# Performance work log

Measured on AMD Instinct MI355X. Metric: run time of the kernel, lower is better.

The kernel has to match this reference:

```python
import jax, jax.numpy as jnp
import numpy as np

H = 0.01      # RK4 step size (parameter.h)
LAM = 1.0     # stage-cost gate penalty
R_COST = 0.1  # scalar control cost R
WMIN, WMAX = -0.01, 0.01  # disturbance range
B, N_STATES, T_STEPS = 8192, 2, 2048

# substituted plant dynamics (parameter.x1_dot / parameter.x2_dot)
def _x1_dot(x1, x2, u):
    return -2.0 * x1 + x2 + u

def _x2_dot(x1, x2, u):
    return x1 - 2.0 * x2 + u

def _rk4_step(x, u):
    # Faithful to RungeKutta.f: k2 == k3 (both evaluated at x2 + h/2)
    x1, x2 = x[0], x[1]
    k1 = jnp.stack([_x1_dot(x1, x2, u), _x2_dot(x1, x2, u)])
    k2 = jnp.stack([_x1_dot(x1, x2 + H / 2, u), _x2_dot(x1, x2 + H / 2, u)])
    k4 = jnp.stack([_x1_dot(x1, x2 + H, u), _x2_dot(x1, x2 + H, u)])
    return x + H * (k1 + 4.0 * k2 + k4) / 6.0  # (k1+2k2+2k3+k4)/6 with k3=k2


def setup_inputs() -> dict:
    key = jax.random.key(0)
    kw, kK, kL, kM, kMo = jax.random.split(key, 5)
    w = jax.random.uniform(kw, (B, N_STATES, T_STEPS), dtype=jnp.float32,
                           minval=WMIN, maxval=WMAX)
    K = 0.1 * jax.random.normal(kK, (1, N_STATES), dtype=jnp.float32)
    L = 0.05 * jax.random.normal(kL, (2 * N_STATES, 2 * N_STATES), dtype=jnp.float32)
    M = 0.05 * jax.random.normal(kM, (1, 2 * N_STATES), dtype=jnp.float32)
    Mo = 0.05 * jax.random.normal(kMo, (1, 1), dtype=jnp.float32)
    return {"w": w, "K": K, "L": L, "M": M, "Mo": Mo}


def reference(w, K, L, M, Mo):
    # w: (B, N, T) disturbances; returns per-sample trajectory cost J, shape (B,)
    Bsz, N, T = w.shape
    dt = w.dtype
    Q = jnp.eye(N, dtype=dt)
    Qf = 10.0 * jnp.eye(N, dtype=dt)
    x0 = jnp.zeros((N,), dtype=dt).at[0].set(1.0)  # xf = 0
    steps = jnp.arange(T)

    def traj_cost(w_b):  # w_b: (N, T)
        def step(carry, inp):
            x, x_hat = carry          # each (N,)
            w_t, i = inp
            z = jnp.concatenate([x, x_hat])            # phi input (2N,)
            phi = z @ L @ z + M[0] @ z + Mo[0, 0]
            delta = jnp.where(i == 0, jnp.asarray(1.0, dt), jax.nn.sigmoid(phi))
            x_hat_n = jnp.where(i == 0, x_hat, delta * x + (1.0 - delta) * x_hat)
            u = K[0] @ x_hat_n                         # control from gated estimate
            x_next = _rk4_step(x, u) + w_t
            u_s = K[0] @ x                             # J uses K @ x[:,i]
            sc = x @ Q @ x + R_COST * u_s * u_s + LAM * delta
            return (x_next, x_hat_n), sc

        (x_T, _), scs = jax.lax.scan(step, (x0, x0), (w_b.T, steps))
        return jnp.sum(scs[: T - 1]) + x_T @ Qf @ x_T

    return jax.vmap(traj_cost)(w)
```

## Files before the change

kernel.cpp:

```cpp
#include <hip/hip_runtime.h>


#define T_STEPS 2048
#define BATCH   8192

__global__ __launch_bounds__(64, 1) void cstr_kernel(
    const float* __restrict__ w,
    const float* __restrict__ K,
    const float* __restrict__ L,
    const float* __restrict__ M,
    const float* __restrict__ Mo,
    float* __restrict__ out)
{
    const int s = blockIdx.x * 64 + (int)threadIdx.x;

    constexpr float Hs = 0.01f;
    constexpr float Ad = 1.0f - 2.0f * Hs;
    constexpr float Rc = 0.1f;
    constexpr float SC = -1.44269504088896340736f;

    const float k1 = K[0], k2 = K[1];

    const float u11 = L[0] * SC;
    const float u12 = (L[1] + L[4]) * SC;
    const float u13 = (L[2] + L[8]) * SC;
    const float u14 = (L[3] + L[12]) * SC;
    const float u22 = L[5] * SC;
    const float u23 = (L[6] + L[9]) * SC;
    const float u24 = (L[7] + L[13]) * SC;
    const float u33 = L[10] * SC;
    const float u34 = (L[11] + L[14]) * SC;
    const float u44 = L[15] * SC;
    const float m1s = M[0] * SC, m2s = M[1] * SC, m3s = M[2] * SC, m4s = M[3] * SC;
    const float c0s = Mo[0] * SC;

    const float hk1 = Hs * k1, hk2 = Hs * k2;
    const float C1v = 0.5f * Hs * Hs;
    const float C21 = -Hs * Hs - C1v;

    float x1 = 1.0f, x2 = 0.0f;
    float h1 = x1, h2 = x2;
    float dx1 = 0.0f, dx2 = 0.0f;
    float phi = __int_as_float(0xff800000u);
    float aA1 = 0.0f, aA2 = 0.0f;
    float aXY = 0.0f;
    float aD  = 0.0f;

    auto step = [&](float w1, float w2, bool cost) {
        float E = __builtin_amdgcn_exp2f(phi);
        float d = __builtin_amdgcn_rcpf(1.0f + E);
        h1 = fmaf(d, dx1, h1);
        h2 = fmaf(d, dx2, h2);
        float t   = fmaf(hk1, h1, C1v);
        float hu1 = fmaf(hk2, h2, t);
        float hu2 = hu1 + C21;
        float b1  = w1 + hu1;
        float b2  = w2 + hu2;
        if (cost) {
            aA1 = fmaf(x1, x1, aA1);
            aA2 = fmaf(x2, x2, aA2);
            aXY = fmaf(x1, x2, aXY);
            aD += d;
        }
        float nx1 = fmaf(Ad, x1, fmaf(Hs, x2, b1));
        float nx2 = fmaf(Ad, x2, fmaf(Hs, x1, b2));
        x1 = nx1; x2 = nx2;
        dx1 = x1 - h1;
        dx2 = x2 - h2;
        float t1 = fmaf(u11, x1, m1s);
        t1 = fmaf(u12, x2, t1);
        t1 = fmaf(u13, h1, t1);
        t1 = fmaf(u14, h2, t1);
        float t2 = fmaf(u22, x2, m2s);
        t2 = fmaf(u23, h1, t2);
        t2 = fmaf(u24, h2, t2);
        float t3 = fmaf(u33, h1, m3s);
        t3 = fmaf(u34, h2, t3);
        float t4 = fmaf(u44, h2, m4s);
        float pp = fmaf(x1, t1, c0s);
        pp = fmaf(x2, t2, pp);
        pp = fmaf(h1, t3, pp);
        phi = fmaf(h2, t4, pp);
    };

    auto chunk = [&](const float4* b0, const float4* b1, bool lastc) {
        #pragma unroll
        for (int q = 0; q < 2; ++q) {
            float4 a = b0[q];
            float4 b = b1[q];
            step(a.x, b.x, true);
            step(a.y, b.y, true);
            step(a.z, b.z, true);
            step(a.w, b.w, !(lastc && (q == 1)));
        }
    };

    const float4* r0 = reinterpret_cast<const float4*>(w + (size_t)s * 2 * T_STEPS);
    const float4* r1 = reinterpret_cast<const float4*>(w + (size_t)s * 2 * T_STEPS + T_STEPS);

    float4 A0[2], A1[2], B0[2], B1[2];
    #pragma unroll
    for (int q = 0; q < 2; ++q) { A0[q] = r0[q];     A1[q] = r1[q]; }
    #pragma unroll
    for (int q = 0; q < 2; ++q) { B0[q] = r0[2 + q]; B1[q] = r1[2 + q]; }

    chunk(A0, A1, false);

    for (int i = 0; i < 127; ++i) {
        const float4* p0 = r0 + (size_t)(2 + 2 * i) * 2;
        const float4* p1 = r1 + (size_t)(2 + 2 * i) * 2;
        #pragma unroll
        for (int q = 0; q < 2; ++q) { A0[q] = p0[q]; A1[q] = p1[q]; }
        chunk(B0, B1, false);
        const float4* q0 = r0 + (size_t)(3 + 2 * i) * 2;
        const float4* q1 = r1 + (size_t)(3 + 2 * i) * 2;
        #pragma unroll
        for (int q = 0; q < 2; ++q) { B0[q] = q0[q]; B1[q] = q1[q]; }
        chunk(A0, A1, false);
    }
    chunk(B0, B1, true);

    float us2 = fmaf(k1 * k1, aA1, fmaf(k2 * k2, aA2, 2.0f * k1 * k2 * aXY));
    float J = aA1 + aA2 + Rc * us2 + aD
            + 10.0f * fmaf(x1, x1, x2 * x2);
    out[s] = J;
}

extern "C" void kernel_launch(void* const* d_in, const int* in_sizes, int n_in,
                              void* d_out, int out_size, void* d_ws, size_t ws_size,
                              hipStream_t stream) {
    const float* w  = (const float*)d_in[0];
    const float* K  = (const float*)d_in[1];
    const float* L  = (const float*)d_in[2];
    const float* M  = (const float*)d_in[3];
    const float* Mo = (const float*)d_in[4];
    float* out = (float*)d_out;

    hipLaunchKernelGGL(cstr_kernel, dim3(BATCH / 64), dim3(64), 0, stream,
                       w, K, L, M, Mo, out);
}
```

Before: 305.7 us.

## Restructure recurrence to compute gate-independent terms off the exp/rcp critical path

Rewrites each step so the quantities that do not depend on the sigmoid gate (the partial state update, the phi partial sums, and their gate-direction corrections) are computed while the exp2/rcp runs. The gate d is then applied through a few final FMAs, and phi is formed as a shallower tree. This targets the serial dependency chain, since only one sequential trajectory runs per thread. It adds more total arithmetic and a running accumulator for K·h plus constants, which may change rounding slightly.

```diff
diff --git a/kernel.cpp b/kernel.cpp
--- a/kernel.cpp
+++ b/kernel.cpp
@@ -31,16 +31,18 @@
     const float u33 = L[10] * SC;
     const float u34 = (L[11] + L[14]) * SC;
     const float u44 = L[15] * SC;
+    const float u1112 = u11 + u12;
     const float m1s = M[0] * SC, m2s = M[1] * SC, m3s = M[2] * SC, m4s = M[3] * SC;
     const float c0s = Mo[0] * SC;
 
     const float hk1 = Hs * k1, hk2 = Hs * k2;
     const float C1v = 0.5f * Hs * Hs;
-    const float C21 = -Hs * Hs - C1v;
+    const float C21 = -1.5f * Hs * Hs;
 
     float x1 = 1.0f, x2 = 0.0f;
     float h1 = x1, h2 = x2;
     float dx1 = 0.0f, dx2 = 0.0f;
+    float kxhC = hk1 + C1v;
     float phi = __int_as_float(0xff800000u);
     float aA1 = 0.0f, aA2 = 0.0f;
     float aXY = 0.0f;
@@ -48,39 +50,53 @@
 
     auto step = [&](float w1, float w2, bool cost) {
         float E = __builtin_amdgcn_exp2f(phi);
+
+        float g   = fmaf(hk1, dx1, hk2 * dx2);
+        float b1  = w1 + kxhC;
+        float w2c = w2 + C21;
+        float b2  = w2c + kxhC;
+        float q1  = fmaf(Ad, x1, fmaf(Hs, x2, b1));
+        float q2  = fmaf(Ad, x2, fmaf(Hs, x1, b2));
+        float t01 = fmaf(u11, q1, m1s);
+        t01 = fmaf(u12, q2, t01);
+        t01 = fmaf(u13, h1, t01);
+        t01 = fmaf(u14, h2, t01);
+        float t02 = fmaf(u22, q2, m2s);
+        t02 = fmaf(u23, h1, t02);
+        t02 = fmaf(u24, h2, t02);
+        float t03 = fmaf(u33, h1, m3s);
+        t03 = fmaf(u34, h2, t03);
+        float t04 = fmaf(u44, h2, m4s);
+        float uv1 = fmaf(u1112, g, fmaf(u13, dx1, u14 * dx2));
+        float uv2 = fmaf(u22, g, fmaf(u23, dx1, u24 * dx2));
+        float uv3 = fmaf(u33, dx1, u34 * dx2);
+        float uv4 = u44 * dx2;
+
         float d = __builtin_amdgcn_rcpf(1.0f + E);
-        h1 = fmaf(d, dx1, h1);
-        h2 = fmaf(d, dx2, h2);
-        float t   = fmaf(hk1, h1, C1v);
-        float hu1 = fmaf(hk2, h2, t);
-        float hu2 = hu1 + C21;
-        float b1  = w1 + hu1;
-        float b2  = w2 + hu2;
+
         if (cost) {
             aA1 = fmaf(x1, x1, aA1);
             aA2 = fmaf(x2, x2, aA2);
             aXY = fmaf(x1, x2, aXY);
             aD += d;
         }
-        float nx1 = fmaf(Ad, x1, fmaf(Hs, x2, b1));
-        float nx2 = fmaf(Ad, x2, fmaf(Hs, x1, b2));
-        x1 = nx1; x2 = nx2;
+        float nx1 = fmaf(d, g, q1);
+        float nx2 = fmaf(d, g, q2);
+        float nh1 = fmaf(d, dx1, h1);
+        float nh2 = fmaf(d, dx2, h2);
+        float nt1 = fmaf(d, uv1, t01);
+        float nt2 = fmaf(d, uv2, t02);
+        float nt3 = fmaf(d, uv3, t03);
+        float nt4 = fmaf(d, uv4, t04);
+        float ma = nx2 * nt2;
+        float mb = fmaf(nh2, nt4, c0s);
+        float pa = fmaf(nx1, nt1, ma);
+        float pb = fmaf(nh1, nt3, mb);
+        phi = pa + pb;
+        kxhC = fmaf(d, g, kxhC);
+        x1 = nx1; x2 = nx2; h1 = nh1; h2 = nh2;
         dx1 = x1 - h1;
         dx2 = x2 - h2;
-        float t1 = fmaf(u11, x1, m1s);
-        t1 = fmaf(u12, x2, t1);
-        t1 = fmaf(u13, h1, t1);
-        t1 = fmaf(u14, h2, t1);
-        float t2 = fmaf(u22, x2, m2s);
-        t2 = fmaf(u23, h1, t2);
-        t2 = fmaf(u24, h2, t2);
-        float t3 = fmaf(u33, h1, m3s);
-        t3 = fmaf(u34, h2, t3);
-        float t4 = fmaf(u44, h2, m4s);
-        float pp = fmaf(x1, t1, c0s);
-        pp = fmaf(x2, t2, pp);
-        pp = fmaf(h1, t3, pp);
-        phi = fmaf(h2, t4, pp);
     };
 
     auto chunk = [&](const float4* b0, const float4* b1, bool lastc) {
```

New measurement: 385.6 us. +26.2%, slower.
